# Kernel tuning notes

Hardware: AMD Instinct MI355X
Metric: run time of the kernel (lower is better)

Reference implementation:

```python
import jax, jax.numpy as jnp
import numpy as np
import math

D_MODEL = 384
D_HEAD = 64
N_HEADS = D_MODEL // D_HEAD  # 6
COND = 768
KSIZE = 7
EPS = 1e-6


def setup_inputs() -> dict:
    key = jax.random.key(0)
    ks = jax.random.split(key, 8)
    n, h, w = 4, 128, 128
    x = jax.random.normal(ks[0], (n, h, w, D_MODEL), jnp.float32)
    pos = jax.random.uniform(ks[1], (n, h, w, 2), jnp.float32)
    cond = jax.random.normal(ks[2], (n, COND), jnp.float32)
    # AdaRMSNorm linear (zero-init in original; small random so it exercises the math)
    w_cond = jax.random.normal(ks[3], (COND, D_MODEL), jnp.float32) * 0.02
    w_qkv = jax.random.normal(ks[4], (D_MODEL, 3 * D_MODEL), jnp.float32) * (D_MODEL ** -0.5)
    scale = jnp.full((N_HEADS,), 10.0, jnp.float32)
    # AxialRoPE freqs: exp(linspace(log(pi), log(10pi), n_heads*dim//4+1)[:-1]).view(dim//4, nh).T
    dim = D_HEAD // 2
    freqs = jnp.exp(jnp.linspace(math.log(math.pi), math.log(10.0 * math.pi),
                                 N_HEADS * (dim // 4) + 1)[:-1])
    freqs = freqs.reshape(dim // 4, N_HEADS).T  # [n_heads, d_head//8]
    w_out = jax.random.normal(ks[5], (D_MODEL, D_MODEL), jnp.float32) * 0.02
    return {"x": x, "pos": pos, "cond": cond, "w_cond": w_cond, "w_qkv": w_qkv,
            "scale": scale, "freqs": freqs, "w_out": w_out}


def rms_norm(x, scale):
    return x * jax.lax.rsqrt(jnp.mean(x * x, axis=-1, keepdims=True) + EPS) * scale


def apply_rotary(x, theta):
    # rotate the first 2*d channels of the head dim, leave the rest untouched
    d = theta.shape[-1]
    x1, x2, x3 = x[..., :d], x[..., d:2 * d], x[..., 2 * d:]
    c, s = jnp.cos(theta), jnp.sin(theta)
    return jnp.concatenate([x1 * c - x2 * s, x2 * c + x1 * s, x3], axis=-1)


def nb_idx(L):
    # NATTEN clamped neighborhood: window start = clip(i - k//2, 0, L-k)
    start = jnp.clip(jnp.arange(L) - KSIZE // 2, 0, L - KSIZE)
    return start[None, :] + jnp.arange(KSIZE)[:, None]  # [KSIZE, L]


def reference(x, pos, cond, w_cond, w_qkv, scale, freqs, w_out):
    n, H, W, _ = x.shape
    skip = x
    # AdaRMSNorm
    x = rms_norm(x, (cond @ w_cond)[:, None, None, :] + 1.0)
    # QKV projection, 'n h w (t nh e) -> t n nh h w e'
    qkv = (x @ w_qkv).reshape(n, H, W, 3, N_HEADS, D_HEAD)
    qkv = jnp.transpose(qkv, (3, 0, 4, 1, 2, 5))
    q, k, v = qkv[0], qkv[1], qkv[2]  # [n, nh, H, W, e]
    # cosine-sim scaling with learned per-head scale
    sq = jnp.sqrt(scale)[:, None, None, None]
    q = q * (sq * jax.lax.rsqrt(jnp.sum(q * q, axis=-1, keepdims=True) + EPS))
    k = k * (sq * jax.lax.rsqrt(jnp.sum(k * k, axis=-1, keepdims=True) + EPS))
    # axial RoPE: theta [n,H,W,nh,d_head//4] per axis -> cat -> movedim(-2,-4)
    th = pos[..., None, 0:1] * freqs
    tw = pos[..., None, 1:2] * freqs
    theta = jnp.moveaxis(jnp.concatenate([th, tw], axis=-1), -2, -4)  # [n,nh,H,W,dd]
    q = apply_rotary(q, theta)
    k = apply_rotary(k, theta)
    # neighborhood attention (na2d_qk / softmax / na2d_av), dilation 1
    ih_all = nb_idx(H)  # [k, H]
    iw_all = nb_idx(W)  # [k, W]
    hh = jnp.repeat(jnp.arange(KSIZE), KSIZE)
    ww = jnp.tile(jnp.arange(KSIZE), KSIZE)
    idx_h = ih_all[hh]  # [k*k, H]
    idx_w = iw_all[ww]  # [k*k, W]

    def qk_step(_, hw):
        ih, iw = hw
        ks_ = k[:, :, ih, :, :][:, :, :, iw, :]  # keys at this window offset
        return None, jnp.einsum('nchwe,nchwe->nchw', q, ks_)

    _, qk = jax.lax.scan(qk_step, None, (idx_h, idx_w))  # [k*k, n, nh, H, W]
    a = jax.nn.softmax(qk, axis=0)  # softmax over the k*k window

    def av_step(acc, inp):
        (ih, iw), at = inp
        vs = v[:, :, ih, :, :][:, :, :, iw, :]
        return acc + at[..., None] * vs, None

    out, _ = jax.lax.scan(av_step, jnp.zeros_like(v), ((idx_h, idx_w), a))
    # 'n nh h w e -> n h w (nh e)'
    out = jnp.transpose(out, (0, 2, 3, 1, 4)).reshape(n, H, W, N_HEADS * D_HEAD)
    return out @ w_out + skip
```

## Files before the change

### kernel.cpp

```cpp
#include <hip/hip_runtime.h>
#include <hip/hip_bf16.h>

#define DM 384
#define NH 6
#define DH 64
#define CD 768
#define NBATCH 4
#define IMH 128
#define IMW 128
#define HEADPIX (IMH*IMW)
#define NPIX (NBATCH*IMH*IMW)
#define PLANE ((size_t)NPIX*DM)
#define KS 7
#define EPSF 1e-6f

typedef __attribute__((ext_vector_type(8))) short bf16x8v;
typedef __attribute__((ext_vector_type(4))) float f32x4v;
typedef __attribute__((ext_vector_type(4))) unsigned short u16x4;

#define GLOAD_LDS16(g, l) __builtin_amdgcn_global_load_lds( \
    (const __attribute__((address_space(1))) void*)(g), \
    (__attribute__((address_space(3))) void*)(l), 16, 0, 0)

__device__ __forceinline__ unsigned short f2bf(float f){
    __hip_bfloat16 h = __float2bfloat16(f);
    return *reinterpret_cast<unsigned short*>(&h);
}

__device__ __forceinline__ bf16x8v frag8(const __hip_bfloat16* base, int row, int kelem){
    int byteoff = row*128 + ((kelem*2) ^ ((row & 7) << 4));
    return *(const bf16x8v*)((const char*)base + byteoff);
}
__device__ __forceinline__ bf16x8v frag512(const char* base, int row, int kelem){
    int byteoff = row*512 + ((kelem*2) ^ ((row & 7) << 4));
    return *(const bf16x8v*)(base + byteoff);
}

__global__ __launch_bounds__(256) void k_cond(const float* __restrict__ cond,
                                              const float* __restrict__ wc,
                                              float* __restrict__ sc){
    __shared__ float red[4][64];
    const int b = blockIdx.x;
    const int n = b / 6, j0 = (b - n*6) * 64;
    const int lane = threadIdx.x & 63, wave = threadIdx.x >> 6;
    const float* cr = cond + n*CD + wave*192;
    const float* wp = wc + (size_t)(wave*192)*DM + j0 + lane;
    float acc = 0.f;
    #pragma unroll 4
    for (int i = 0; i < 192; ++i) acc += cr[i] * wp[(size_t)i*DM];
    red[wave][lane] = acc;
    __syncthreads();
    if (threadIdx.x < 64) {
        float s = red[0][lane] + red[1][lane] + red[2][lane] + red[3][lane];
        sc[n*DM + j0 + lane] = s + 1.0f;
    }
}

__global__ __launch_bounds__(256) void k_xscale(const float* __restrict__ x,
                                                const float* __restrict__ sc,
                                                __hip_bfloat16* __restrict__ xb){
    int row  = blockIdx.x*4 + (threadIdx.x>>6);
    int lane = threadIdx.x & 63;
    int n    = row >> 14;
    const float* xr  = x + (size_t)row*DM;
    const float* scp = sc + n*DM;
    float v[6];
    float s = 0.f;
    #pragma unroll
    for (int i=0;i<6;++i){ v[i] = xr[i*64+lane]; s += v[i]*v[i]; }
    #pragma unroll
    for (int o=32;o;o>>=1) s += __shfl_xor(s,o);
    float r = rsqrtf(s*(1.0f/DM) + EPSF);
    #pragma unroll
    for (int i=0;i<6;++i)
        xb[(size_t)row*DM + i*64+lane] = __float2bfloat16(v[i]*r*scp[i*64+lane]);
}

__global__ void k_cvtwq(const float* __restrict__ wq, __hip_bfloat16* __restrict__ wqb){
    int id = blockIdx.x*256 + threadIdx.x;
    if (id >= 3*DM*DM) return;
    int nn = id / DM, kk = id - nn*DM;
    wqb[id] = __float2bfloat16(wq[(size_t)kk*(3*DM) + nn]);
}
__global__ void k_cvtwo(const float* __restrict__ wo, __hip_bfloat16* __restrict__ wob){
    int id = blockIdx.x*256 + threadIdx.x;
    if (id >= DM*DM) return;
    int nn = id / DM, kk = id - nn*DM;
    wob[id] = __float2bfloat16(wo[(size_t)kk*DM + nn]);
}

__global__ __launch_bounds__(256) void k_qkv_mfma(
    const __hip_bfloat16* __restrict__ xb, const __hip_bfloat16* __restrict__ wqb,
    const float* __restrict__ pos, const float* __restrict__ freqs,
    const float* __restrict__ scale, __hip_bfloat16* __restrict__ qkv)
{
    __shared__ char As[2*16384];
    __shared__ char Bs[2*16384];
    const int t    = threadIdx.x;
    const int lane = t & 63;
    const int wave = t >> 6;
    const int swzb = (blockIdx.x & 7)*576 + (blockIdx.x >> 3);
    const int jb = swzb % 9;
    const int mb = swzb / 9;
    const int j0 = jb*128, m0 = mb*128;
    const int n  = m0 >> 14;
    const int wr = (wave >> 1) * 64;
    const int wc = (wave & 1) * 64;
    const int fr = lane & 15;
    const int fg = lane >> 4;

    f32x4v acc[4][4] = {};

#define STAGE_QKV(buf, k0) \
    { _Pragma("unroll") \
      for (int i = 0; i < 4; ++i) { \
        int off = (i*256 + t) * 8; \
        int row = off >> 6; \
        int col = (off & 63) ^ ((row & 7) << 3); \
        GLOAD_LDS16(xb  + (size_t)(m0 + row)*DM + (k0) + col, \
                    As + (buf)*16384 + (i*256 + (wave<<6))*16); \
        GLOAD_LDS16(wqb + (size_t)(j0 + row)*DM + (k0) + col, \
                    Bs + (buf)*16384 + (i*256 + (wave<<6))*16); \
      } }

    STAGE_QKV(0, 0)
    #pragma unroll
    for (int kt = 0; kt < 6; ++kt) {
        const int cur = kt & 1;
        if (kt < 5) {
            STAGE_QKV(cur ^ 1, (kt+1)*64)
            asm volatile("s_waitcnt vmcnt(8)" ::: "memory");
        } else {
            asm volatile("s_waitcnt vmcnt(0)" ::: "memory");
        }
        asm volatile("s_barrier" ::: "memory");
        const __hip_bfloat16* Ab = (const __hip_bfloat16*)(As + cur*16384);
        const __hip_bfloat16* Bb = (const __hip_bfloat16*)(Bs + cur*16384);
        #pragma unroll
        for (int kk = 0; kk < 64; kk += 32) {
            bf16x8v af[4], bfr[4];
            #pragma unroll
            for (int i = 0; i < 4; ++i) af[i]  = frag8(Ab, wr + i*16 + fr, kk + fg*8);
            #pragma unroll
            for (int i = 0; i < 4; ++i) bfr[i] = frag8(Bb, wc + i*16 + fr, kk + fg*8);
            #pragma unroll
            for (int i = 0; i < 4; ++i)
            #pragma unroll
            for (int j = 0; j < 4; ++j)
                acc[i][j] = __builtin_amdgcn_mfma_f32_16x16x32_bf16(bfr[i], af[j], acc[i][j], 0, 0, 0);
        }
        asm volatile("s_barrier" ::: "memory");
    }
#undef STAGE_QKV

    const int t_ = jb / 3;
    const int pj = jb - t_*3;
    const int c  = pj*2 + (wc >> 6);
    const size_t hbase = (size_t)t_*PLANE + (((size_t)(n*NH + c)*HEADPIX) << 6);

    if (t_ < 2) {
        const float sq = sqrtf(scale[c]);
        const float4 f4 = *(const float4*)(freqs + c*8 + ((fg & 1) << 2));
        float fqv[4] = {f4.x, f4.y, f4.z, f4.w};
        #pragma unroll
        for (int ni = 0; ni < 4; ++ni) {
            int m = m0 + wr + ni*16 + fr;
            float ss = 0.f;
            #pragma unroll
            for (int i = 0; i < 4; ++i)
                #pragma unroll
                for (int r = 0; r < 4; ++r) ss += acc[i][ni][r]*acc[i][ni][r];
            ss += __shfl_xor(ss, 16);
            ss += __shfl_xor(ss, 32);
            float rn = sq * rsqrtf(ss + EPSF);
            float2 pp = *(const float2*)(pos + (size_t)m*2);
            float pc = (fg < 2) ? pp.x : pp.y;
            u16x4 o0, o1, o2, o3;
            #pragma unroll
            for (int r = 0; r < 4; ++r) {
                float th = pc * fqv[r];
                float ct = __cosf(th), st = __sinf(th);
                float a0 = acc[0][ni][r]*rn, a1 = acc[1][ni][r]*rn;
                o0[r] = f2bf(a0*ct - a1*st);
                o1[r] = f2bf(a1*ct + a0*st);
                o2[r] = f2bf(acc[2][ni][r]*rn);
                o3[r] = f2bf(acc[3][ni][r]*rn);
            }
            size_t base = hbase + ((size_t)(m & (HEADPIX-1)) << 6) + (fg << 2);
            *(u16x4*)(qkv + base     ) = o0;
            *(u16x4*)(qkv + base + 16) = o1;
            *(u16x4*)(qkv + base + 32) = o2;
            *(u16x4*)(qkv + base + 48) = o3;
        }
    } else {
        #pragma unroll
        for (int ni = 0; ni < 4; ++ni) {
            int m = m0 + wr + ni*16 + fr;
            size_t base = hbase + ((size_t)(m & (HEADPIX-1)) << 6) + (fg << 2);
            #pragma unroll
            for (int i = 0; i < 4; ++i) {
                u16x4 pk;
                #pragma unroll
                for (int r = 0; r < 4; ++r) pk[r] = f2bf(acc[i][ni][r]);
                *(u16x4*)(qkv + base + i*16) = pk;
            }
        }
    }
}

__global__ __launch_bounds__(256) void k_attn2(
    const __hip_bfloat16* __restrict__ q, const __hip_bfloat16* __restrict__ kbuf,
    const __hip_bfloat16* __restrict__ vbuf, __hip_bfloat16* __restrict__ attn)
{
    __shared__ char smem[65536];
    char* KP = smem;
    char* VT = smem + 32768;

    const int t    = threadIdx.x;
    const int lane = t & 63;
    const int wave = t >> 6;
    const int fr   = lane & 15;
    const int fg   = lane >> 4;

    const int tile = blockIdx.x;
    const int n6c  = blockIdx.y;
    const int h0 = (tile >> 4) << 3;
    const int w0 = (tile & 15) << 3;
    const int nn = n6c / NH;
    const int cc = n6c - nn*NH;

    const size_t pixbase = (size_t)n6c << 14;
    const __hip_bfloat16* qp = q    + (pixbase << 6);
    const __hip_bfloat16* kp = kbuf + (pixbase << 6);
    const __hip_bfloat16* vp = vbuf + (pixbase << 6);

    const int u0h = min(max(h0-3,0), IMH-7);
    const int u0w = min(max(w0-3,0), IMW-7);

    #pragma unroll
    for (int it = 0; it < 7; ++it) {
        if (it < 6 || t < 128) {
            int chunk = it*256 + t;
            int key  = chunk >> 3;
            int part = chunk & 7;
            int keyc = min(key, 195);
            int uh = keyc / 14;
            int uw = keyc - uh*14;
            int kh = min(u0h + uh, IMH-1);
            int kw = min(u0w + uw, IMW-1);
            GLOAD_LDS16(kp + (((size_t)kh*IMW + kw) << 6) + ((part ^ (key & 7)) << 3),
                        KP + (it*256 + (wave<<6))*16);
        }
    }
    {
        int key = (wave<<6) + lane;
        bool kv = key < 196;
        int keyc = min(key, 195);
        int uh = keyc / 14;
        int uw = keyc - uh*14;
        int kh = min(u0h + uh, IMH-1);
        int kw = min(u0w + uw, IMW-1);
        const __hip_bfloat16* vrow = vp + (((size_t)kh*IMW + kw) << 6);
        #pragma unroll
        for (int jb = 0; jb < 8; ++jb) {
            uint4 vv = {0u,0u,0u,0u};
            if (kv) vv = *(const uint4*)(vrow + jb*8);
            unsigned vals[4] = {vv.x, vv.y, vv.z, vv.w};
            #pragma unroll
            for (int mm = 0; mm < 4; ++mm) {
                int d0 = jb*8 + mm*2;
                *(ushort*)(VT + d0*512     + ((key*2) ^ (( d0     & 7) << 4))) = (ushort)(vals[mm] & 0xFFFFu);
                *(ushort*)(VT + (d0+1)*512 + ((key*2) ^ (((d0+1) & 7) << 4))) = (ushort)(vals[mm] >> 16);
            }
        }
    }
    const int q_l = (wave<<4) + fr;
    const int qh = h0 + (q_l >> 3), qw = w0 + (q_l & 7);
    const __hip_bfloat16* qrow = qp + (((size_t)qh*IMW + qw) << 6);
    bf16x8v aq0 = *(const bf16x8v*)(qrow + fg*8);
    bf16x8v aq1 = *(const bf16x8v*)(qrow + 32 + fg*8);

    int loh[4], low_[4];
    #pragma unroll
    for (int r = 0; r < 4; ++r) {
        int qr  = (wave<<4) + fg*4 + r;
        int qhr = h0 + (qr >> 3), qwr = w0 + (qr & 7);
        loh[r]  = min(max(qhr-3,0), IMH-7) - u0h;
        low_[r] = min(max(qwr-3,0), IMW-7) - u0w;
    }

    __syncthreads();

    f32x4v acc_s[13];
    #pragma unroll
    for (int nf = 0; nf < 13; ++nf) {
        bf16x8v b0 = frag8((const __hip_bfloat16*)KP, nf*16 + fr, fg*8);
        bf16x8v b1 = frag8((const __hip_bfloat16*)KP, nf*16 + fr, 32 + fg*8);
        f32x4v s = {0.f,0.f,0.f,0.f};
        s = __builtin_amdgcn_mfma_f32_16x16x32_bf16(aq0, b0, s, 0, 0, 0);
        s = __builtin_amdgcn_mfma_f32_16x16x32_bf16(aq1, b1, s, 0, 0, 0);
        acc_s[nf] = s;
    }

    float rs[4] = {0.f,0.f,0.f,0.f};
    #pragma unroll
    for (int nf = 0; nf < 13; ++nf) {
        int key = nf*16 + fr;
        int uh = key / 14;
        int uw = key - uh*14;
        bool kin = key < 196;
        #pragma unroll
        for (int r = 0; r < 4; ++r) {
            bool ok = kin && ((unsigned)(uh - loh[r]) <= 6u) && ((unsigned)(uw - low_[r]) <= 6u);
            float pv = ok ? __expf(acc_s[nf][r]) : 0.f;
            acc_s[nf][r] = pv;
            rs[r] += pv;
        }
    }
    #pragma unroll
    for (int o = 1; o < 16; o <<= 1) {
        #pragma unroll
        for (int r = 0; r < 4; ++r) rs[r] += __shfl_xor(rs[r], o);
    }
    float rinv[4];
    #pragma unroll
    for (int r = 0; r < 4; ++r) rinv[r] = 1.0f / rs[r];

    __syncthreads();

    #pragma unroll
    for (int nf = 0; nf < 14; ++nf) {
        int key = nf*16 + fr;
        #pragma unroll
        for (int r = 0; r < 4; ++r) {
            int qr = (wave<<4) + fg*4 + r;
            float pv = (nf < 13) ? acc_s[nf][r] : 0.f;
            *(__hip_bfloat16*)(KP + qr*512 + ((key*2) ^ ((qr & 7) << 4))) = __float2bfloat16(pv);
        }
    }
    __syncthreads();

    f32x4v acc_o[4] = {};
    #pragma unroll
    for (int kst = 0; kst < 7; ++kst) {
        bf16x8v a = frag512(KP, (wave<<4) + fr, kst*32 + fg*8);
        #pragma unroll
        for (int nf = 0; nf < 4; ++nf) {
            bf16x8v b = frag512(VT, nf*16 + fr, kst*32 + fg*8);
            acc_o[nf] = __builtin_amdgcn_mfma_f32_16x16x32_bf16(a, b, acc_o[nf], 0, 0, 0);
        }
    }

    #pragma unroll
    for (int nf = 0; nf < 4; ++nf) {
        int d = cc*64 + nf*16 + fr;
        #pragma unroll
        for (int r = 0; r < 4; ++r) {
            int qr  = (wave<<4) + fg*4 + r;
            int qhr = h0 + (qr >> 3), qwr = w0 + (qr & 7);
            size_t pix = ((size_t)nn << 14) + (size_t)qhr*IMW + qwr;
            attn[pix*DM + d] = __float2bfloat16(acc_o[nf][r] * rinv[r]);
        }
    }
}

__global__ __launch_bounds__(256) void k_out_mfma(
    const __hip_bfloat16* __restrict__ attn, const __hip_bfloat16* __restrict__ wob,
    const float* __restrict__ xin, float* __restrict__ out)
{
    __shared__ char As[2*16384];
    __shared__ char Bs[2*16384];
    const int t    = threadIdx.x;
    const int lane = t & 63;
    const int wave = t >> 6;
    const int swzb = (blockIdx.x & 7)*192 + (blockIdx.x >> 3);
    const int jb = swzb % 3;
    const int mb = swzb / 3;
    const int j0 = jb*128, m0 = mb*128;
    const int wr = (wave >> 1) * 64;
    const int wc = (wave & 1) * 64;
    const int fr = lane & 15;
    const int fg = lane >> 4;

    f32x4v acc[4][4] = {};

#define STAGE_OUT(buf, k0) \
    { _Pragma("unroll") \
      for (int i = 0; i < 4; ++i) { \
        int off = (i*256 + t) * 8; \
        int row = off >> 6; \
        int col = (off & 63) ^ ((row & 7) << 3); \
        GLOAD_LDS16(attn + (size_t)(m0 + row)*DM + (k0) + col, \
                    As + (buf)*16384 + (i*256 + (wave<<6))*16); \
        GLOAD_LDS16(wob  + (size_t)(j0 + row)*DM + (k0) + col, \
                    Bs + (buf)*16384 + (i*256 + (wave<<6))*16); \
      } }

    STAGE_OUT(0, 0)
    #pragma unroll
    for (int kt = 0; kt < 6; ++kt) {
        const int cur = kt & 1;
        if (kt < 5) {
            STAGE_OUT(cur ^ 1, (kt+1)*64)
            asm volatile("s_waitcnt vmcnt(8)" ::: "memory");
        } else {
            asm volatile("s_waitcnt vmcnt(0)" ::: "memory");
        }
        asm volatile("s_barrier" ::: "memory");
        const __hip_bfloat16* Ab = (const __hip_bfloat16*)(As + cur*16384);
        const __hip_bfloat16* Bb = (const __hip_bfloat16*)(Bs + cur*16384);
        #pragma unroll
        for (int kk = 0; kk < 64; kk += 32) {
            bf16x8v af[4], bfr[4];
            #pragma unroll
            for (int i = 0; i < 4; ++i) af[i]  = frag8(Ab, wr + i*16 + fr, kk + fg*8);
            #pragma unroll
            for (int i = 0; i < 4; ++i) bfr[i] = frag8(Bb, wc + i*16 + fr, kk + fg*8);
            #pragma unroll
            for (int i = 0; i < 4; ++i)
            #pragma unroll
            for (int j = 0; j < 4; ++j)
                acc[i][j] = __builtin_amdgcn_mfma_f32_16x16x32_bf16(bfr[i], af[j], acc[i][j], 0, 0, 0);
        }
        asm volatile("s_barrier" ::: "memory");
    }
#undef STAGE_OUT

    #pragma unroll
    for (int i = 0; i < 4; ++i) {
        int jg = j0 + wc + i*16 + (fg<<2);
        #pragma unroll
        for (int ni = 0; ni < 4; ++ni) {
            int m = m0 + wr + ni*16 + fr;
            size_t idx = (size_t)m*DM + jg;
            float4 xv = *(const float4*)(xin + idx);
            float4 ov;
            ov.x = acc[i][ni][0] + xv.x;
            ov.y = acc[i][ni][1] + xv.y;
            ov.z = acc[i][ni][2] + xv.z;
            ov.w = acc[i][ni][3] + xv.w;
            *(float4*)(out + idx) = ov;
        }
    }
}

extern "C" void kernel_launch(void* const* d_in, const int* in_sizes, int n_in,
                              void* d_out, int out_size, void* d_ws, size_t ws_size,
                              hipStream_t stream) {
    const float* x      = (const float*)d_in[0];
    const float* pos    = (const float*)d_in[1];
    const float* cond   = (const float*)d_in[2];
    const float* w_cond = (const float*)d_in[3];
    const float* w_qkv  = (const float*)d_in[4];
    const float* scale  = (const float*)d_in[5];
    const float* freqs  = (const float*)d_in[6];
    const float* w_out  = (const float*)d_in[7];
    float* out = (float*)d_out;

    char* ws = (char*)d_ws;
    __hip_bfloat16* xb   = (__hip_bfloat16*)ws;
    __hip_bfloat16* attn = (__hip_bfloat16*)ws;
    __hip_bfloat16* qkv  = (__hip_bfloat16*)(ws + 50331648);
    float* s_cond = (float*)(ws + 201326592);
    __hip_bfloat16* wqb = (__hip_bfloat16*)(ws + 201332736);
    __hip_bfloat16* qb = qkv;
    __hip_bfloat16* kb = qkv + PLANE;
    __hip_bfloat16* vb = qkv + 2*PLANE;
    __hip_bfloat16* wob = qkv;

    k_cvtwq<<<1728, 256, 0, stream>>>(w_qkv, wqb);
    k_cond<<<24, 256, 0, stream>>>(cond, w_cond, s_cond);
    k_xscale<<<NPIX/4, 256, 0, stream>>>(x, s_cond, xb);
    k_qkv_mfma<<<4608, 256, 0, stream>>>(xb, wqb, pos, freqs, scale, qkv);
    k_attn2<<<dim3(256, 24), 256, 0, stream>>>(qb, kb, vb, attn);
    k_cvtwo<<<576, 256, 0, stream>>>(w_out, wob);
    k_out_mfma<<<1536, 256, 0, stream>>>(attn, wob, x, out);
}
```

Measured before the change: 299.9 us.

## Load GEMM weights into registers and stage V via async LDS with transpose reads

In both GEMM kernels the weight (B) tiles now go straight from global memory into double-buffered registers instead of through LDS. This halves shared-memory use and drops the LDS round trip for B, at the cost of extra VGPRs and uncoalesced 16-byte loads. In the attention kernel the key window is padded to a 14x16 grid so index math becomes shifts. V is copied asynchronously into LDS with global_load_lds and read with ds_read_b64_tr_b16 transpose loads, replacing the scalar per-element transpose scatter. The padding adds one extra 16-key MFMA block.

```diff
diff --git a/kernel.cpp b/kernel.cpp
--- a/kernel.cpp
+++ b/kernel.cpp
@@ -15,6 +15,7 @@
 #define EPSF 1e-6f
 
 typedef __attribute__((ext_vector_type(8))) short bf16x8v;
+typedef __attribute__((ext_vector_type(4))) short bf16x4v;
 typedef __attribute__((ext_vector_type(4))) float f32x4v;
 typedef __attribute__((ext_vector_type(4))) unsigned short u16x4;
 
@@ -22,9 +23,18 @@
     (const __attribute__((address_space(1))) void*)(g), \
     (__attribute__((address_space(3))) void*)(l), 16, 0, 0)
 
+#define TR64(dst, p, imm) asm volatile("ds_read_b64_tr_b16 %0, %1 offset:" #imm \
+    : "=v"(dst) : "v"((const __attribute__((address_space(3))) char*)(p)))
+
 __device__ __forceinline__ unsigned short f2bf(float f){
     __hip_bfloat16 h = __float2bfloat16(f);
     return *reinterpret_cast<unsigned short*>(&h);
+}
+__device__ __forceinline__ bf16x8v cat8(bf16x4v lo, bf16x4v hi){
+    bf16x8v r;
+    r[0]=lo[0]; r[1]=lo[1]; r[2]=lo[2]; r[3]=lo[3];
+    r[4]=hi[0]; r[5]=hi[1]; r[6]=hi[2]; r[7]=hi[3];
+    return r;
 }
 
 __device__ __forceinline__ bf16x8v frag8(const __hip_bfloat16* base, int row, int kelem){
@@ -95,7 +105,6 @@
     const float* __restrict__ scale, __hip_bfloat16* __restrict__ qkv)
 {
     __shared__ char As[2*16384];
-    __shared__ char Bs[2*16384];
     const int t    = threadIdx.x;
     const int lane = t & 63;
     const int wave = t >> 6;
@@ -111,47 +120,53 @@
 
     f32x4v acc[4][4] = {};
 
-#define STAGE_QKV(buf, k0) \
+#define STAGE_A(buf, k0) \
     { _Pragma("unroll") \
       for (int i = 0; i < 4; ++i) { \
         int off = (i*256 + t) * 8; \
         int row = off >> 6; \
         int col = (off & 63) ^ ((row & 7) << 3); \
-        GLOAD_LDS16(xb  + (size_t)(m0 + row)*DM + (k0) + col, \
+        GLOAD_LDS16(xb + (size_t)(m0 + row)*DM + (k0) + col, \
                     As + (buf)*16384 + (i*256 + (wave<<6))*16); \
-        GLOAD_LDS16(wqb + (size_t)(j0 + row)*DM + (k0) + col, \
-                    Bs + (buf)*16384 + (i*256 + (wave<<6))*16); \
       } }
-
-    STAGE_QKV(0, 0)
+#define LOADB_Q(bb, k0) \
+    { _Pragma("unroll") \
+      for (int i = 0; i < 4; ++i) { \
+        const __hip_bfloat16* bp = wqb + (size_t)(j0 + wc + i*16 + fr)*DM + (k0) + fg*8; \
+        bb[i]   = *(const bf16x8v*)bp; \
+        bb[4+i] = *(const bf16x8v*)(bp + 32); \
+      } }
+
+    bf16x8v breg[2][8];
+    LOADB_Q(breg[0], 0)
+    STAGE_A(0, 0)
     #pragma unroll
     for (int kt = 0; kt < 6; ++kt) {
         const int cur = kt & 1;
         if (kt < 5) {
-            STAGE_QKV(cur ^ 1, (kt+1)*64)
-            asm volatile("s_waitcnt vmcnt(8)" ::: "memory");
+            STAGE_A(cur ^ 1, (kt+1)*64)
+            LOADB_Q(breg[cur ^ 1], (kt+1)*64)
+            asm volatile("s_waitcnt vmcnt(12)" ::: "memory");
         } else {
             asm volatile("s_waitcnt vmcnt(0)" ::: "memory");
         }
         asm volatile("s_barrier" ::: "memory");
         const __hip_bfloat16* Ab = (const __hip_bfloat16*)(As + cur*16384);
-        const __hip_bfloat16* Bb = (const __hip_bfloat16*)(Bs + cur*16384);
         #pragma unroll
         for (int kk = 0; kk < 64; kk += 32) {
-            bf16x8v af[4], bfr[4];
-            #pragma unroll
-            for (int i = 0; i < 4; ++i) af[i]  = frag8(Ab, wr + i*16 + fr, kk + fg*8);
-            #pragma unroll
-            for (int i = 0; i < 4; ++i) bfr[i] = frag8(Bb, wc + i*16 + fr, kk + fg*8);
+            bf16x8v af[4];
+            #pragma unroll
+            for (int j = 0; j < 4; ++j) af[j] = frag8(Ab, wr + j*16 + fr, kk + fg*8);
             #pragma unroll
             for (int i = 0; i < 4; ++i)
             #pragma unroll
             for (int j = 0; j < 4; ++j)
-                acc[i][j] = __builtin_amdgcn_mfma_f32_16x16x32_bf16(bfr[i], af[j], acc[i][j], 0, 0, 0);
+                acc[i][j] = __builtin_amdgcn_mfma_f32_16x16x32_bf16(breg[cur][(kk>>5)*4 + i], af[j], acc[i][j], 0, 0, 0);
         }
         asm volatile("s_barrier" ::: "memory");
     }
-#undef STAGE_QKV
+#undef STAGE_A
+#undef LOADB_Q
 
     const int t_ = jb / 3;
     const int pj = jb - t_*3;
@@ -212,7 +227,7 @@
     const __hip_bfloat16* __restrict__ q, const __hip_bfloat16* __restrict__ kbuf,
     const __hip_bfloat16* __restrict__ vbuf, __hip_bfloat16* __restrict__ attn)
 {
-    __shared__ char smem[65536];
+    __shared__ char smem[61440];
     char* KP = smem;
     char* VT = smem + 32768;
 
@@ -239,40 +254,25 @@
 
     #pragma unroll
     for (int it = 0; it < 7; ++it) {
-        if (it < 6 || t < 128) {
-            int chunk = it*256 + t;
-            int key  = chunk >> 3;
-            int part = chunk & 7;
-            int keyc = min(key, 195);
-            int uh = keyc / 14;
-            int uw = keyc - uh*14;
-            int kh = min(u0h + uh, IMH-1);
-            int kw = min(u0w + uw, IMW-1);
-            GLOAD_LDS16(kp + (((size_t)kh*IMW + kw) << 6) + ((part ^ (key & 7)) << 3),
-                        KP + (it*256 + (wave<<6))*16);
-        }
-    }
-    {
-        int key = (wave<<6) + lane;
-        bool kv = key < 196;
-        int keyc = min(key, 195);
-        int uh = keyc / 14;
-        int uw = keyc - uh*14;
-        int kh = min(u0h + uh, IMH-1);
-        int kw = min(u0w + uw, IMW-1);
-        const __hip_bfloat16* vrow = vp + (((size_t)kh*IMW + kw) << 6);
-        #pragma unroll
-        for (int jb = 0; jb < 8; ++jb) {
-            uint4 vv = {0u,0u,0u,0u};
-            if (kv) vv = *(const uint4*)(vrow + jb*8);
-            unsigned vals[4] = {vv.x, vv.y, vv.z, vv.w};
-            #pragma unroll
-            for (int mm = 0; mm < 4; ++mm) {
-                int d0 = jb*8 + mm*2;
-                *(ushort*)(VT + d0*512     + ((key*2) ^ (( d0     & 7) << 4))) = (ushort)(vals[mm] & 0xFFFFu);
-                *(ushort*)(VT + (d0+1)*512 + ((key*2) ^ (((d0+1) & 7) << 4))) = (ushort)(vals[mm] >> 16);
-            }
-        }
+        int chunk = it*256 + t;
+        int key  = chunk >> 3;
+        int part = chunk & 7;
+        int kh = min(u0h + (key >> 4), IMH-1);
+        int kw = min(u0w + (key & 15), IMW-1);
+        GLOAD_LDS16(kp + (((size_t)kh*IMW + kw) << 6) + ((part ^ (key & 7)) << 3),
+                    KP + (it*256 + (wave<<6))*16);
+    }
+    #pragma unroll
+    for (int it = 0; it < 7; ++it) {
+        int chunk = it*256 + t;
+        int keyq = chunk >> 5;
+        int rem  = chunk & 31;
+        int key  = (keyq << 2) + ((rem >> 1) & 3);
+        int d0   = ((rem >> 3) << 4) + ((chunk & 1) << 3);
+        int kh = min(u0h + (key >> 4), IMH-1);
+        int kw = min(u0w + (key & 15), IMW-1);
+        GLOAD_LDS16(vp + (((size_t)kh*IMW + kw) << 6) + d0,
+                    VT + (it*256 + (wave<<6))*16);
     }
     const int q_l = (wave<<4) + fr;
     const int qh = h0 + (q_l >> 3), qw = w0 + (q_l & 7);
@@ -291,9 +291,9 @@
 
     __syncthreads();
 
-    f32x4v acc_s[13];
-    #pragma unroll
-    for (int nf = 0; nf < 13; ++nf) {
+    f32x4v acc_s[14];
+    #pragma unroll
+    for (int nf = 0; nf < 14; ++nf) {
         bf16x8v b0 = frag8((const __hip_bfloat16*)KP, nf*16 + fr, fg*8);
         bf16x8v b1 = frag8((const __hip_bfloat16*)KP, nf*16 + fr, 32 + fg*8);
         f32x4v s = {0.f,0.f,0.f,0.f};
@@ -304,14 +304,13 @@
 
     float rs[4] = {0.f,0.f,0.f,0.f};
     #pragma unroll
-    for (int nf = 0; nf < 13; ++nf) {
+    for (int nf = 0; nf < 14; ++nf) {
         int key = nf*16 + fr;
-        int uh = key / 14;
-        int uw = key - uh*14;
-        bool kin = key < 196;
+        int uh = key >> 4;
+        int uw = key & 15;
         #pragma unroll
         for (int r = 0; r < 4; ++r) {
-            bool ok = kin && ((unsigned)(uh - loh[r]) <= 6u) && ((unsigned)(uw - low_[r]) <= 6u);
+            bool ok = ((unsigned)(uh - loh[r]) <= 6u) && ((unsigned)(uw - low_[r]) <= 6u);
             float pv = ok ? __expf(acc_s[nf][r]) : 0.f;
             acc_s[nf][r] = pv;
             rs[r] += pv;
@@ -334,21 +333,28 @@
         #pragma unroll
         for (int r = 0; r < 4; ++r) {
             int qr = (wave<<4) + fg*4 + r;
-            float pv = (nf < 13) ? acc_s[nf][r] : 0.f;
-            *(__hip_bfloat16*)(KP + qr*512 + ((key*2) ^ ((qr & 7) << 4))) = __float2bfloat16(pv);
+            *(__hip_bfloat16*)(KP + qr*512 + ((key*2) ^ ((qr & 7) << 4))) = __float2bfloat16(acc_s[nf][r]);
         }
     }
     __syncthreads();
 
     f32x4v acc_o[4] = {};
+    const char* vlane = VT + ((lane >> 4) << 10) + ((lane & 15) << 3);
     #pragma unroll
     for (int kst = 0; kst < 7; ++kst) {
         bf16x8v a = frag512(KP, (wave<<4) + fr, kst*32 + fg*8);
-        #pragma unroll
-        for (int nf = 0; nf < 4; ++nf) {
-            bf16x8v b = frag512(VT, nf*16 + fr, kst*32 + fg*8);
-            acc_o[nf] = __builtin_amdgcn_mfma_f32_16x16x32_bf16(a, b, acc_o[nf], 0, 0, 0);
-        }
+        const char* vk = vlane + kst*4096;
+        bf16x4v t0a, t0b, t1a, t1b, t2a, t2b, t3a, t3b;
+        TR64(t0a, vk,   0); TR64(t0b, vk, 512);
+        TR64(t1a, vk, 128); TR64(t1b, vk, 640);
+        TR64(t2a, vk, 256); TR64(t2b, vk, 768);
+        TR64(t3a, vk, 384); TR64(t3b, vk, 896);
+        asm volatile("s_waitcnt lgkmcnt(0)" ::: "memory");
+        __builtin_amdgcn_sched_barrier(0);
+        acc_o[0] = __builtin_amdgcn_mfma_f32_16x16x32_bf16(a, cat8(t0a,t0b), acc_o[0], 0, 0, 0);
+        acc_o[1] = __builtin_amdgcn_mfma_f32_16x16x32_bf16(a, cat8(t1a,t1b), acc_o[1], 0, 0, 0);
+        acc_o[2] = __builtin_amdgcn_mfma_f32_16x16x32_bf16(a, cat8(t2a,t2b), acc_o[2], 0, 0, 0);
+        acc_o[3] = __builtin_amdgcn_mfma_f32_16x16x32_bf16(a, cat8(t3a,t3b), acc_o[3], 0, 0, 0);
     }
 
     #pragma unroll
@@ -369,7 +375,6 @@
     const float* __restrict__ xin, float* __restrict__ out)
 {
     __shared__ char As[2*16384];
-    __shared__ char Bs[2*16384];
     const int t    = threadIdx.x;
     const int lane = t & 63;
     const int wave = t >> 6;
@@ -384,7 +389,7 @@
 
     f32x4v acc[4][4] = {};
 
-#define STAGE_OUT(buf, k0) \
+#define STAGE_A(buf, k0) \
     { _Pragma("unroll") \
       for (int i = 0; i < 4; ++i) { \
         int off = (i*256 + t) * 8; \
@@ -392,39 +397,45 @@
         int col = (off & 63) ^ ((row & 7) << 3); \
         GLOAD_LDS16(attn + (size_t)(m0 + row)*DM + (k0) + col, \
                     As + (buf)*16384 + (i*256 + (wave<<6))*16); \
-        GLOAD_LDS16(wob  + (size_t)(j0 + row)*DM + (k0) + col, \
-                    Bs + (buf)*16384 + (i*256 + (wave<<6))*16); \
       } }
-
-    STAGE_OUT(0, 0)
+#define LOADB_O(bb, k0) \
+    { _Pragma("unroll") \
+      for (int i = 0; i < 4; ++i) { \
+        const __hip_bfloat16* bp = wob + (size_t)(j0 + wc + i*16 + fr)*DM + (k0) + fg*8; \
+        bb[i]   = *(const bf16x8v*)bp; \
+        bb[4+i] = *(const bf16x8v*)(bp + 32); \
+      } }
+
+    bf16x8v breg[2][8];
+    LOADB_O(breg[0], 0)
+    STAGE_A(0, 0)
     #pragma unroll
     for (int kt = 0; kt < 6; ++kt) {
         const int cur = kt & 1;
         if (kt < 5) {
-            STAGE_OUT(cur ^ 1, (kt+1)*64)
-            asm volatile("s_waitcnt vmcnt(8)" ::: "memory");
+            STAGE_A(cur ^ 1, (kt+1)*64)
+            LOADB_O(breg[cur ^ 1], (kt+1)*64)
+            asm volatile("s_waitcnt vmcnt(12)" ::: "memory");
         } else {
             asm volatile("s_waitcnt vmcnt(0)" ::: "memory");
         }
         asm volatile("s_barrier" ::: "memory");
         const __hip_bfloat16* Ab = (const __hip_bfloat16*)(As + cur*16384);
-        const __hip_bfloat16* Bb = (const __hip_bfloat16*)(Bs + cur*16384);
         #pragma unroll
         for (int kk = 0; kk < 64; kk += 32) {
-            bf16x8v af[4], bfr[4];
-            #pragma unroll
-            for (int i = 0; i < 4; ++i) af[i]  = frag8(Ab, wr + i*16 + fr, kk + fg*8);
-            #pragma unroll
-            for (int i = 0; i < 4; ++i) bfr[i] = frag8(Bb, wc + i*16 + fr, kk + fg*8);
+            bf16x8v af[4];
+            #pragma unroll
+            for (int j = 0; j < 4; ++j) af[j] = frag8(Ab, wr + j*16 + fr, kk + fg*8);
             #pragma unroll
             for (int i = 0; i < 4; ++i)
             #pragma unroll
             for (int j = 0; j < 4; ++j)
-                acc[i][j] = __builtin_amdgcn_mfma_f32_16x16x32_bf16(bfr[i], af[j], acc[i][j], 0, 0, 0);
+                acc[i][j] = __builtin_amdgcn_mfma_f32_16x16x32_bf16(breg[cur][(kk>>5)*4 + i], af[j], acc[i][j], 0, 0, 0);
         }
         asm volatile("s_barrier" ::: "memory");
     }
-#undef STAGE_OUT
+#undef STAGE_A
+#undef LOADB_O
 
     #pragma unroll
     for (int i = 0; i < 4; ++i) {
```

Result: slower. 345.4 us (+15.2%).
